# Performance work log

Measured on AMD Instinct MI355X. Metric: run time of the kernel, lower is better.

## Reference

```python
import jax, jax.numpy as jnp
import numpy as np

B, Q, K, H = 8, 512, 512, 64
KEY_D, QUERY_D, VAL_D = 256, 256, 256

def setup_inputs() -> dict:
    key = jax.random.key(0)
    ks = jax.random.split(key, 6)
    return {
        "key": jax.random.normal(ks[0], (B, K, KEY_D), dtype=jnp.float32),
        "query": jax.random.normal(ks[1], (B, Q, QUERY_D), dtype=jnp.float32),
        "value": jax.random.normal(ks[2], (B, K, VAL_D), dtype=jnp.float32),
        "mask": jnp.zeros((B, Q, K), dtype=bool),
        "W_k": jax.random.normal(ks[3], (KEY_D, H), dtype=jnp.float32) / np.sqrt(KEY_D),
        "W_q": jax.random.normal(ks[4], (QUERY_D, H), dtype=jnp.float32) / np.sqrt(QUERY_D),
        "w_v": jax.random.normal(ks[5], (H,), dtype=jnp.float32) / np.sqrt(H),
    }

def reference(key, query, value, mask, W_k, W_q, w_v):
    q = query @ W_q                      # [B, Q, H]
    k = key @ W_k                        # [B, K, H]
    feats = jnp.tanh(q[:, :, None, :] + k[:, None, :, :])  # [B, Q, K, H]
    score = jnp.einsum('bqkh,h->bqk', feats, w_v)           # [B, Q, K]
    score = jnp.where(mask, -jnp.inf, score)
    attn = jax.nn.softmax(score, axis=-1)                   # [B, Q, K]
    return jnp.einsum('bqk,bkd->bqd', attn, value)          # [B, Q, VAL_D]
```

## Files before the change

### kernel.cpp

```cpp
#include <hip/hip_runtime.h>
#include <math.h>

#define NB 8
#define NQ 512
#define NK 512
#define NH 64
#define ND 256
#define QT 8

typedef float f32x2 __attribute__((ext_vector_type(2)));
typedef float f32x4 __attribute__((ext_vector_type(4)));

#define EXP2(x) __builtin_amdgcn_exp2f(x)
#define RCP(x)  __builtin_amdgcn_rcpf(x)
#define SCALE2 2.8853900817779268f
#define LOG2E  1.4426950408889634f

static __device__ __forceinline__ f32x2 sp2(float v) { return (f32x2){v, v}; }
static __device__ __forceinline__ f32x2 fma2(f32x2 a, f32x2 b, f32x2 c) {
    return __builtin_elementwise_fma(a, b, c);
}
static __device__ __forceinline__ f32x2 mk2(float x, float y) {
    return (f32x2){x, y};
}

static __device__ __forceinline__ void score4(
    const f32x2 k0, const f32x2 k1, const f32x2 k2, const f32x2 k3,
    const f32x4 eqv, const f32x4 fqv, const float w01a, const float w01b,
    f32x2& acc)
{
    const f32x2 t0 = k0 * eqv.x;
    const f32x2 t1 = k1 * eqv.y;
    const f32x2 ua = t0 + t1 + 1.0f;
    const f32x2 da = fma2(t0, t1, ua);
    f32x2 na = fma2(k0, sp2(fqv.x), sp2(w01a));
    na = fma2(k1, sp2(fqv.y), na);
    const f32x2 t2 = k2 * eqv.z;
    const f32x2 t3 = k3 * eqv.w;
    const f32x2 ub = t2 + t3 + 1.0f;
    const f32x2 db = fma2(t2, t3, ub);
    f32x2 nb = fma2(k2, sp2(fqv.z), sp2(w01b));
    nb = fma2(k3, sp2(fqv.w), nb);
    const f32x2 D = da * db;
    f32x2 N = na * db;
    N = fma2(nb, da, N);
    const f32x2 rD = mk2(RCP(D.x), RCP(D.y));
    acc = fma2(N, rD, acc);
}

__global__ __launch_bounds__(256, 4) void proj_kernel(
    const float* __restrict__ query, const float* __restrict__ key,
    const float* __restrict__ Wq, const float* __restrict__ Wk,
    const float* __restrict__ w_v,
    float* __restrict__ qside, float* __restrict__ Ekp,
    float* __restrict__ w01g, float* __restrict__ wsumg)
{
    __shared__ __align__(16) float insT[ND][12];
    __shared__ float pacc[3][4][NH][2];
    const int t = threadIdx.x;
    const bool isK = blockIdx.x >= 512;
    const float* __restrict__ in = isK ? key : query;
    const float* __restrict__ W  = isK ? Wk : Wq;
    const int rowbase = (blockIdx.x & 511) * 8;

    {
        const int r = t & 7, c = (t >> 3) * 8;
        const float* src = in + (size_t)(rowbase + r) * ND + c;
        const f32x4 v0 = *(const f32x4*)src;
        const f32x4 v1 = *(const f32x4*)(src + 4);
        insT[c + 0][r] = v0.x; insT[c + 1][r] = v0.y;
        insT[c + 2][r] = v0.z; insT[c + 3][r] = v0.w;
        insT[c + 4][r] = v1.x; insT[c + 5][r] = v1.y;
        insT[c + 6][r] = v1.z; insT[c + 7][r] = v1.w;
    }
    __syncthreads();

    const int lane = t & 63;
    const int w    = t >> 6;
    const int d0   = w * 64;

    f32x2 acc[4] = {{0.f,0.f},{0.f,0.f},{0.f,0.f},{0.f,0.f}};
    for (int dd = 0; dd < 64; ++dd) {
        const int d = d0 + dd;
        const float wv = W[(size_t)d * NH + lane];
        const f32x4 rA = *(const f32x4*)&insT[d][0];
        const f32x4 rB = *(const f32x4*)&insT[d][4];
        acc[0] = fma2(mk2(rA.x, rA.y), sp2(wv), acc[0]);
        acc[1] = fma2(mk2(rA.z, rA.w), sp2(wv), acc[1]);
        acc[2] = fma2(mk2(rB.x, rB.y), sp2(wv), acc[2]);
        acc[3] = fma2(mk2(rB.z, rB.w), sp2(wv), acc[3]);
    }
    if (w > 0) {
        #pragma unroll
        for (int rp = 0; rp < 4; ++rp)
            *(f32x2*)&pacc[w - 1][rp][lane][0] = acc[rp];
    }
    __syncthreads();
    if (w == 0) {
        float e[8];
        #pragma unroll
        for (int rp = 0; rp < 4; ++rp) {
            f32x2 a = acc[rp];
            a += *(const f32x2*)&pacc[0][rp][lane][0];
            a += *(const f32x2*)&pacc[1][rp][lane][0];
            a += *(const f32x2*)&pacc[2][rp][lane][0];
            e[2 * rp] = a.x; e[2 * rp + 1] = a.y;
        }
        #pragma unroll
        for (int j = 0; j < 8; ++j) {
            const float x = fminf(fmaxf(e[j] * SCALE2, -30.f), 30.f);
            e[j] = EXP2(x);
        }
        if (!isK) {
            const float wx = w_v[lane ^ 1];
            #pragma unroll
            for (int j = 0; j < 8; ++j) {
                const int g = rowbase + j;
                float* dst = qside + ((size_t)g * 16 + (lane >> 2)) * 8 + (lane & 3);
                dst[0] = e[j];
                dst[4] = wx * e[j];
            }
        } else {
            #pragma unroll
            for (int j = 0; j < 8; ++j) {
                const int g = rowbase + j;
                const int bb = g >> 9, kk = g & 511;
                Ekp[((size_t)bb * NH + lane) * NK + kk] = e[j];
            }
        }
    }
    if (blockIdx.x == 0) {
        if (t < 32) w01g[t] = w_v[2 * t] + w_v[2 * t + 1];
        if (t == 64) {
            float s = 0.f;
            for (int h = 0; h < NH; ++h) s += w_v[h];
            wsumg[0] = s;
        }
    }
}

__global__ __launch_bounds__(512, 4) void attn_kernel(
    const float* __restrict__ qside, const float* __restrict__ Ekp,
    const float* __restrict__ value, const unsigned char* __restrict__ mask,
    const float* __restrict__ w01g, const float* __restrict__ wsumg,
    float* __restrict__ out)
{
    __shared__ __align__(16) float ps[QT][NK];
    __shared__ __align__(16) float reds[QT][4];
    __shared__ __align__(16) float pacc[3][4][ND];

    const int t    = threadIdx.x;
    const int lane = t & 63;
    const int w    = t >> 6;
    const int bid  = ((int)(blockIdx.x & 7) << 6) | ((int)blockIdx.x >> 3);
    const int b    = bid >> 6;
    const int q0   = (bid & 63) * QT;
    const int rh   = __builtin_amdgcn_readfirstlane(t >> 8);
    const int kp   = t & 255;

    const float wsumL = wsumg[0] * LOG2E;
    const float* __restrict__ qs  = qside + (size_t)(b * NQ + q0 + rh * 4) * 128;
    const float* __restrict__ ekc = Ekp + (size_t)b * NH * NK + 2 * kp;

    f32x2 eA[4], eB[4];
    #pragma unroll
    for (int j = 0; j < 4; ++j) eA[j] = *(const f32x2*)&ekc[(size_t)j * NK];
    #pragma unroll
    for (int j = 0; j < 4; ++j) eB[j] = *(const f32x2*)&ekc[(size_t)(4 + j) * NK];

    f32x2 acc[4] = {{0.f,0.f},{0.f,0.f},{0.f,0.f},{0.f,0.f}};

    for (int hc = 0; hc < 16; hc += 2) {
        {
            const f32x2 k0 = eA[0], k1 = eA[1], k2 = eA[2], k3 = eA[3];
            if (hc + 2 < 16) {
                #pragma unroll
                for (int j = 0; j < 4; ++j)
                    eA[j] = *(const f32x2*)&ekc[(size_t)(4 * (hc + 2) + j) * NK];
            }
            const float wa = w01g[2 * hc], wb = w01g[2 * hc + 1];
            #pragma unroll
            for (int r = 0; r < 4; ++r) {
                const f32x4 eqv = *(const f32x4*)&qs[r * 128 + hc * 8];
                const f32x4 fqv = *(const f32x4*)&qs[r * 128 + hc * 8 + 4];
                score4(k0, k1, k2, k3, eqv, fqv, wa, wb, acc[r]);
            }
        }
        {
            const f32x2 k0 = eB[0], k1 = eB[1], k2 = eB[2], k3 = eB[3];
            if (hc + 3 < 16) {
                #pragma unroll
                for (int j = 0; j < 4; ++j)
                    eB[j] = *(const f32x2*)&ekc[(size_t)(4 * (hc + 3) + j) * NK];
            }
            const float wa = w01g[2 * hc + 2], wb = w01g[2 * hc + 3];
            #pragma unroll
            for (int r = 0; r < 4; ++r) {
                const f32x4 eqv = *(const f32x4*)&qs[r * 128 + (hc + 1) * 8];
                const f32x4 fqv = *(const f32x4*)&qs[r * 128 + (hc + 1) * 8 + 4];
                score4(k0, k1, k2, k3, eqv, fqv, wa, wb, acc[r]);
            }
        }
    }

    const unsigned char* __restrict__ mb =
        mask + (size_t)(b * NQ + q0 + rh * 4) * NK + 2 * kp;
    f32x2 p[4];
    #pragma unroll
    for (int r = 0; r < 4; ++r) {
        f32x2 arg = fma2(acc[r], sp2(-2.f * LOG2E), sp2(wsumL));
        const unsigned short m = *(const unsigned short*)(mb + (size_t)r * NK);
        if (m & 0x00ff) arg.x = -__builtin_inff();
        if (m & 0xff00) arg.y = -__builtin_inff();
        p[r] = mk2(EXP2(arg.x), EXP2(arg.y));
    }

    #pragma unroll
    for (int r = 0; r < 4; ++r) {
        float s = p[r].x + p[r].y;
        #pragma unroll
        for (int off = 32; off; off >>= 1) s += __shfl_xor(s, off, 64);
        if (lane == 0) reds[rh * 4 + r][w & 3] = s;
    }
    __syncthreads();
    #pragma unroll
    for (int r = 0; r < 4; ++r) {
        const f32x4 sv = *(const f32x4*)&reds[rh * 4 + r][0];
        const float gsum = (sv.x + sv.y) + (sv.z + sv.w);
        p[r] = p[r] * RCP(gsum);
        *(f32x2*)&ps[rh * 4 + r][2 * kp] = p[r];
    }
    __syncthreads();

    const int kq   = w >> 1;
    const int dh   = w & 1;
    const int dcol = dh * 128 + 2 * lane;
    f32x2 a[QT];
    #pragma unroll
    for (int r = 0; r < QT; ++r) a[r] = (f32x2){0.f, 0.f};

    const float* __restrict__ vb = value + ((size_t)b * NK + kq * 128) * ND + dcol;
    for (int kk = 0; kk < 128; kk += 4) {
        const int kbase = kq * 128 + kk;
        const f32x2 v0 = *(const f32x2*)&vb[(size_t)(kk + 0) * ND];
        const f32x2 v1 = *(const f32x2*)&vb[(size_t)(kk + 1) * ND];
        const f32x2 v2 = *(const f32x2*)&vb[(size_t)(kk + 2) * ND];
        const f32x2 v3 = *(const f32x2*)&vb[(size_t)(kk + 3) * ND];
        #pragma unroll
        for (int half = 0; half < 2; ++half) {
            #pragma unroll
            for (int rr = 0; rr < 4; ++rr) {
                const int r = half * 4 + rr;
                const f32x4 P = *(const f32x4*)&ps[r][kbase];
                a[r] = fma2(sp2(P.x), v0, a[r]);
                a[r] = fma2(sp2(P.y), v1, a[r]);
                a[r] = fma2(sp2(P.z), v2, a[r]);
                a[r] = fma2(sp2(P.w), v3, a[r]);
            }
        }
    }

    if (kq > 0) {
        #pragma unroll
        for (int r = 0; r < 4; ++r)
            *(f32x2*)&pacc[kq - 1][r][dcol] = a[r];
    }
    __syncthreads();
    if (kq == 0) {
        #pragma unroll
        for (int r = 0; r < 4; ++r) {
            f32x2 v = a[r];
            v += *(const f32x2*)&pacc[0][r][dcol];
            v += *(const f32x2*)&pacc[1][r][dcol];
            v += *(const f32x2*)&pacc[2][r][dcol];
            *(f32x2*)&out[(size_t)(b * NQ + q0 + r) * ND + dcol] = v;
        }
    }
    __syncthreads();
    if (kq > 0) {
        #pragma unroll
        for (int r = 0; r < 4; ++r)
            *(f32x2*)&pacc[kq - 1][r][dcol] = a[4 + r];
    }
    __syncthreads();
    if (kq == 0) {
        #pragma unroll
        for (int r = 0; r < 4; ++r) {
            f32x2 v = a[4 + r];
            v += *(const f32x2*)&pacc[0][r][dcol];
            v += *(const f32x2*)&pacc[1][r][dcol];
            v += *(const f32x2*)&pacc[2][r][dcol];
            *(f32x2*)&out[(size_t)(b * NQ + q0 + 4 + r) * ND + dcol] = v;
        }
    }
}

extern "C" void kernel_launch(void* const* d_in, const int* in_sizes, int n_in,
                              void* d_out, int out_size, void* d_ws, size_t ws_size,
                              hipStream_t stream) {
    const float* key   = (const float*)d_in[0];
    const float* query = (const float*)d_in[1];
    const float* value = (const float*)d_in[2];
    const unsigned char* mask = (const unsigned char*)d_in[3];
    const float* Wk  = (const float*)d_in[4];
    const float* Wq  = (const float*)d_in[5];
    const float* w_v = (const float*)d_in[6];
    float* out = (float*)d_out;

    float* Ekp   = (float*)d_ws;
    float* qside = Ekp + (size_t)NB * NH * NK;
    float* w01g  = qside + (size_t)NB * NQ * 128;
    float* wsumg = w01g + 32;

    proj_kernel<<<1024, 256, 0, stream>>>(query, key, Wq, Wk, w_v,
                                          qside, Ekp, w01g, wsumg);
    attn_kernel<<<NB * (NQ / QT), 512, 0, stream>>>(qside, Ekp, value, mask,
                                                    w01g, wsumg, out);
}
```

Baseline: 48.25 us.

## Split attention into score and fp16 MFMA PV kernels with transposed half-precision values

The fused attention kernel is split in two. A score kernel writes normalized probabilities as fp16 to a global workspace. A new pv_kernel computes P·V with 16x16x32 f16 MFMA instructions instead of scalar packed FMAs. The projection kernel gains extra blocks that convert value to fp16 and transpose it into a K-contiguous layout for the MFMA B operand. This trades fp32 vector ALU work for matrix cores, at the cost of an extra launch, a global round trip for P, and reduced precision in P and V.

```diff
diff --git a/kernel.cpp b/kernel.cpp
--- a/kernel.cpp
+++ b/kernel.cpp
@@ -10,6 +10,8 @@
 
 typedef float f32x2 __attribute__((ext_vector_type(2)));
 typedef float f32x4 __attribute__((ext_vector_type(4)));
+typedef _Float16 f16x2 __attribute__((ext_vector_type(2)));
+typedef _Float16 f16x8 __attribute__((ext_vector_type(8)));
 
 #define EXP2(x) __builtin_amdgcn_exp2f(x)
 #define RCP(x)  __builtin_amdgcn_rcpf(x)
@@ -22,6 +24,13 @@
 }
 static __device__ __forceinline__ f32x2 mk2(float x, float y) {
     return (f32x2){x, y};
+}
+static __device__ __forceinline__ f16x2 cvt2h(float a, float b) {
+#if __has_builtin(__builtin_amdgcn_cvt_pkrtz)
+    return __builtin_bit_cast(f16x2, __builtin_amdgcn_cvt_pkrtz(a, b));
+#else
+    return (f16x2){(_Float16)a, (_Float16)b};
+#endif
 }
 
 static __device__ __forceinline__ void score4(
@@ -50,14 +59,35 @@
 
 __global__ __launch_bounds__(256, 4) void proj_kernel(
     const float* __restrict__ query, const float* __restrict__ key,
+    const float* __restrict__ value,
     const float* __restrict__ Wq, const float* __restrict__ Wk,
     const float* __restrict__ w_v,
     float* __restrict__ qside, float* __restrict__ Ekp,
-    float* __restrict__ w01g, float* __restrict__ wsumg)
+    float* __restrict__ w01g, float* __restrict__ wsumg,
+    _Float16* __restrict__ VhT)
 {
+    const int t = threadIdx.x;
+
+    if (blockIdx.x >= 1024) {
+        const int vbase = ((int)blockIdx.x - 1024) * 8;
+        const int bb = vbase >> 9, k0 = vbase & 511;
+        const int d = t;
+        const float* __restrict__ vsrc = value + ((size_t)bb * NK + k0) * ND + d;
+        float v[8];
+        #pragma unroll
+        for (int j = 0; j < 8; ++j) v[j] = vsrc[(size_t)j * ND];
+        f16x8 hv;
+        #pragma unroll
+        for (int j = 0; j < 4; ++j) {
+            const f16x2 h = cvt2h(v[2 * j], v[2 * j + 1]);
+            hv[2 * j] = h.x; hv[2 * j + 1] = h.y;
+        }
+        *(f16x8*)&VhT[((size_t)bb * ND + d) * NK + k0] = hv;
+        return;
+    }
+
     __shared__ __align__(16) float insT[ND][12];
     __shared__ float pacc[3][4][NH][2];
-    const int t = threadIdx.x;
     const bool isK = blockIdx.x >= 512;
     const float* __restrict__ in = isK ? key : query;
     const float* __restrict__ W  = isK ? Wk : Wq;
@@ -139,15 +169,13 @@
     }
 }
 
-__global__ __launch_bounds__(512, 4) void attn_kernel(
+__global__ __launch_bounds__(512, 4) void score_kernel(
     const float* __restrict__ qside, const float* __restrict__ Ekp,
-    const float* __restrict__ value, const unsigned char* __restrict__ mask,
+    const unsigned char* __restrict__ mask,
     const float* __restrict__ w01g, const float* __restrict__ wsumg,
-    float* __restrict__ out)
+    _Float16* __restrict__ Ph)
 {
-    __shared__ __align__(16) float ps[QT][NK];
-    __shared__ __align__(16) float reds[QT][4];
-    __shared__ __align__(16) float pacc[3][4][ND];
+    __shared__ float reds[QT][4];
 
     const int t    = threadIdx.x;
     const int lane = t & 63;
@@ -226,72 +254,56 @@
     #pragma unroll
     for (int r = 0; r < 4; ++r) {
         const f32x4 sv = *(const f32x4*)&reds[rh * 4 + r][0];
-        const float gsum = (sv.x + sv.y) + (sv.z + sv.w);
-        p[r] = p[r] * RCP(gsum);
-        *(f32x2*)&ps[rh * 4 + r][2 * kp] = p[r];
-    }
-    __syncthreads();
-
-    const int kq   = w >> 1;
-    const int dh   = w & 1;
-    const int dcol = dh * 128 + 2 * lane;
-    f32x2 a[QT];
-    #pragma unroll
-    for (int r = 0; r < QT; ++r) a[r] = (f32x2){0.f, 0.f};
-
-    const float* __restrict__ vb = value + ((size_t)b * NK + kq * 128) * ND + dcol;
-    for (int kk = 0; kk < 128; kk += 4) {
-        const int kbase = kq * 128 + kk;
-        const f32x2 v0 = *(const f32x2*)&vb[(size_t)(kk + 0) * ND];
-        const f32x2 v1 = *(const f32x2*)&vb[(size_t)(kk + 1) * ND];
-        const f32x2 v2 = *(const f32x2*)&vb[(size_t)(kk + 2) * ND];
-        const f32x2 v3 = *(const f32x2*)&vb[(size_t)(kk + 3) * ND];
-        #pragma unroll
-        for (int half = 0; half < 2; ++half) {
-            #pragma unroll
-            for (int rr = 0; rr < 4; ++rr) {
-                const int r = half * 4 + rr;
-                const f32x4 P = *(const f32x4*)&ps[r][kbase];
-                a[r] = fma2(sp2(P.x), v0, a[r]);
-                a[r] = fma2(sp2(P.y), v1, a[r]);
-                a[r] = fma2(sp2(P.z), v2, a[r]);
-                a[r] = fma2(sp2(P.w), v3, a[r]);
-            }
-        }
-    }
-
-    if (kq > 0) {
-        #pragma unroll
-        for (int r = 0; r < 4; ++r)
-            *(f32x2*)&pacc[kq - 1][r][dcol] = a[r];
-    }
-    __syncthreads();
-    if (kq == 0) {
-        #pragma unroll
-        for (int r = 0; r < 4; ++r) {
-            f32x2 v = a[r];
-            v += *(const f32x2*)&pacc[0][r][dcol];
-            v += *(const f32x2*)&pacc[1][r][dcol];
-            v += *(const f32x2*)&pacc[2][r][dcol];
-            *(f32x2*)&out[(size_t)(b * NQ + q0 + r) * ND + dcol] = v;
-        }
-    }
-    __syncthreads();
-    if (kq > 0) {
-        #pragma unroll
-        for (int r = 0; r < 4; ++r)
-            *(f32x2*)&pacc[kq - 1][r][dcol] = a[4 + r];
-    }
-    __syncthreads();
-    if (kq == 0) {
-        #pragma unroll
-        for (int r = 0; r < 4; ++r) {
-            f32x2 v = a[4 + r];
-            v += *(const f32x2*)&pacc[0][r][dcol];
-            v += *(const f32x2*)&pacc[1][r][dcol];
-            v += *(const f32x2*)&pacc[2][r][dcol];
-            *(f32x2*)&out[(size_t)(b * NQ + q0 + 4 + r) * ND + dcol] = v;
-        }
+        const float rin = RCP((sv.x + sv.y) + (sv.z + sv.w));
+        const f32x2 pn = p[r] * rin;
+        *(f16x2*)&Ph[(size_t)(b * NQ + q0 + rh * 4 + r) * NK + 2 * kp] =
+            cvt2h(pn.x, pn.y);
+    }
+}
+
+__global__ __launch_bounds__(512, 4) void pv_kernel(
+    const _Float16* __restrict__ Ph, const _Float16* __restrict__ VhT,
+    float* __restrict__ out)
+{
+    const int t    = threadIdx.x;
+    const int lane = t & 63;
+    const int w    = t >> 6;
+    const int bid  = ((int)(blockIdx.x & 7) << 5) | ((int)blockIdx.x >> 3);
+    const int b    = bid >> 5;
+    const int q0   = (bid & 31) * 16;
+    const int ln   = lane & 15;
+    const int kg   = lane >> 4;
+
+    const _Float16* __restrict__ pA =
+        Ph + (size_t)(b * NQ + q0 + ln) * NK + kg * 8;
+    const _Float16* __restrict__ pB0 =
+        VhT + (size_t)(b * ND + w * 32 + ln) * NK + kg * 8;
+    const _Float16* __restrict__ pB1 = pB0 + (size_t)16 * NK;
+
+    f32x4 c0 = {0.f, 0.f, 0.f, 0.f}, c1 = {0.f, 0.f, 0.f, 0.f};
+    f16x8 a  = *(const f16x8*)pA;
+    f16x8 b0 = *(const f16x8*)pB0;
+    f16x8 b1 = *(const f16x8*)pB1;
+
+    #pragma unroll
+    for (int s = 0; s < 16; ++s) {
+        f16x8 an = a, b0n = b0, b1n = b1;
+        if (s < 15) {
+            an  = *(const f16x8*)(pA  + 32 * (s + 1));
+            b0n = *(const f16x8*)(pB0 + 32 * (s + 1));
+            b1n = *(const f16x8*)(pB1 + 32 * (s + 1));
+        }
+        c0 = __builtin_amdgcn_mfma_f32_16x16x32_f16(a, b0, c0, 0, 0, 0);
+        c1 = __builtin_amdgcn_mfma_f32_16x16x32_f16(a, b1, c1, 0, 0, 0);
+        a = an; b0 = b0n; b1 = b1n;
+    }
+
+    #pragma unroll
+    for (int i = 0; i < 4; ++i) {
+        float* __restrict__ o =
+            out + (size_t)(b * NQ + q0 + 4 * kg + i) * ND + w * 32 + ln;
+        o[0]  = c0[i];
+        o[16] = c1[i];
     }
 }
 
@@ -311,9 +323,11 @@
     float* qside = Ekp + (size_t)NB * NH * NK;
     float* w01g  = qside + (size_t)NB * NQ * 128;
     float* wsumg = w01g + 32;
-
-    proj_kernel<<<1024, 256, 0, stream>>>(query, key, Wq, Wk, w_v,
-                                          qside, Ekp, w01g, wsumg);
-    attn_kernel<<<NB * (NQ / QT), 512, 0, stream>>>(qside, Ekp, value, mask,
-                                                    w01g, wsumg, out);
-}
+    _Float16* Ph  = (_Float16*)(w01g + 64);
+    _Float16* VhT = Ph + (size_t)NB * NQ * NK;
+
+    proj_kernel<<<1536, 256, 0, stream>>>(query, key, value, Wq, Wk, w_v,
+                                          qside, Ekp, w01g, wsumg, VhT);
+    score_kernel<<<512, 512, 0, stream>>>(qside, Ekp, mask, w01g, wsumg, Ph);
+    pv_kernel<<<256, 512, 0, stream>>>(Ph, VhT, out);
+}
```

Measured after the change: 46.44 us. -3.8%, faster.
